# Optimization experiments

Hardware: AMD Instinct MI355X
Metric: run time of the kernel (lower is better)

## Reference

```python
import jax, jax.numpy as jnp
import numpy as np
import math

D = 768      # n_embd
NH = 12      # n_head
L = 4        # n_layer
E = 8        # num_experts
K = 2        # top_k
V = 50257    # vocab
H = 4 * D    # ffn hidden
MOE_LAYERS = (1, 3)


def _ln(x, g, b):
    m = x.mean(-1, keepdims=True)
    v = ((x - m) ** 2).mean(-1, keepdims=True)
    return (x - m) * jax.lax.rsqrt(v + 1e-5) * g + b


def setup_inputs() -> dict:
    key = jax.random.key(0)
    ks = iter(jax.random.split(key, 32))
    s = 0.02

    def rnd(shape):
        return jax.random.normal(next(ks), shape, dtype=jnp.float32) * s

    inp = {
        "x": jax.random.randint(next(ks), (2, 512), 0, V),
        "emb": rnd((V, D)),                       # tied embedding / output projection
        "wqkv": rnd((L, 3 * D, D)), "bqkv": jnp.zeros((L, 3 * D)),
        "wo": rnd((L, D, D)), "bo": jnp.zeros((L, D)),
        "ln1g": jnp.ones((L, D)), "ln1b": jnp.zeros((L, D)),
        "ln2g": jnp.ones((L, D)), "ln2b": jnp.zeros((L, D)),
        "sw1": rnd((2, H, D)), "sb1": jnp.zeros((2, H)),   # dense FFN layers (0, 2)
        "sw2": rnd((2, D, H)), "sb2": jnp.zeros((2, D)),
        "gw": rnd((2, E, D)),                              # router weights (layers 1, 3)
        "mw1": rnd((2, E, H, D)), "mb1": jnp.zeros((2, E, H)),
        "mw2": rnd((2, E, D, H)), "mb2": jnp.zeros((2, E, D)),
        "lnfg": jnp.ones((D,)), "lnfb": jnp.zeros((D,)),
    }
    return inp


def reference(x, emb, wqkv, bqkv, wo, bo, ln1g, ln1b, ln2g, ln2b,
              sw1, sb1, sw2, sb2, gw, mw1, mb1, mw2, mb2, lnfg, lnfb):
    b, t = x.shape
    dh = D // NH

    h = emb[x]  # [b,t,d]
    # sinusoidal positional encoding
    pos = jnp.arange(t, dtype=jnp.float32)[:, None]
    div = jnp.exp(jnp.arange(0, D, 2, dtype=jnp.float32) * (-math.log(10000.0) / D))
    pe = jnp.stack([jnp.sin(pos * div), jnp.cos(pos * div)], axis=-1).reshape(t, D)
    h = h + pe[None]

    # causal mask: query i cannot attend to key j > i
    neg = jnp.asarray(-jnp.inf, dtype=h.dtype)
    mask = jnp.where(jnp.arange(t)[None, :] > jnp.arange(t)[:, None], neg, 0.0)

    std_i = 0
    moe_i = 0
    for i in range(L):
        # pre-norm self-attention
        xn = _ln(h, ln1g[i], ln1b[i])
        qkv = xn @ wqkv[i].T + bqkv[i]          # [b,t,3d]
        q, k, v = jnp.split(qkv, 3, axis=-1)

        def heads(z):
            return z.reshape(b, t, NH, dh).transpose(0, 2, 1, 3)  # [b,nh,t,dh]

        q, k, v = heads(q), heads(k), heads(v)
        sc = jnp.einsum('bhqd,bhkd->bhqk', q, k) / math.sqrt(dh) + mask
        a = jax.nn.softmax(sc, axis=-1)
        o = jnp.einsum('bhqk,bhkd->bhqd', a, v).transpose(0, 2, 1, 3).reshape(b, t, D)
        h = h + o @ wo[i].T + bo[i]

        # pre-norm FFN (dense or MoE)
        xn = _ln(h, ln2g[i], ln2b[i])
        if i in MOE_LAYERS:
            T = b * t
            xf = xn.reshape(T, D)
            gl = xf @ gw[moe_i].T                      # router logits [T,E]
            probs = jax.nn.softmax(gl, axis=-1)
            topv, topi = jax.lax.top_k(probs, K)       # [T,K]
            w = topv / topv.sum(-1, keepdims=True)     # renormalized top-k gates
            cw = jnp.zeros_like(probs).at[jnp.arange(T)[:, None], topi].set(w)  # [T,E]
            he = jax.nn.gelu(jnp.einsum('td,ehd->teh', xf, mw1[moe_i]) + mb1[moe_i],
                             approximate=False)        # [T,E,H]
            ye = jnp.einsum('teh,edh->ted', he, mw2[moe_i]) + mb2[moe_i]        # [T,E,D]
            ff = jnp.einsum('ted,te->td', ye, cw).reshape(b, t, D)
            moe_i += 1
        else:
            ff = jax.nn.gelu(xn @ sw1[std_i].T + sb1[std_i], approximate=False) @ sw2[std_i].T + sb2[std_i]
            std_i += 1
        h = h + ff

    h = _ln(h, lnfg, lnfb)
    logits = h @ emb.T  # tied output projection, [b,t,V]
    return logits
```

## Files before the change

### kernel.cpp

```cpp
#include <hip/hip_runtime.h>
#include <hip/hip_bf16.h>
#include <cstdint>
#include <cstddef>

#define Dm   768
#define NHm  12
#define Lm   4
#define Em   8
#define Vm   50257
#define Hm   3072
#define Tm   512
#define Bm   2
#define NT   (Bm*Tm)
#define NAS  (NT*2)

typedef float f32x4 __attribute__((ext_vector_type(4)));
typedef short bf16x8 __attribute__((ext_vector_type(8)));

__device__ __forceinline__ float gelu_exact(float x) {
    return 0.5f * x * (1.0f + erff(x * 0.70710678118654752440f));
}

__device__ __forceinline__ unsigned short f2bf(float f) {
    __hip_bfloat16 h = __float2bfloat16(f);
// ... 111 lines not shown
    if (valid) {
        const float4* s4 = reinterpret_cast<const float4*>(src);
        #pragma unroll
        for (int q = 0; q < 4; ++q) {
            float4 f = s4[q];
            float vv[4] = {f.x, f.y, f.z, f.w};
            #pragma unroll
            for (int j = 0; j < 4; ++j) {
                int idx = q * 4 + j;
                unsigned short hb = f2bf(vv[j]);
                unsigned short lb = f2bf(vv[j] - bf2f_bits(hb));
                if (idx < 8) { h0.s[idx] = hb; l0.s[idx] = lb; }
                else         { h1.s[idx - 8] = hb; l1.s[idx - 8] = lb; }
            }
        }
    } else {
        h0.v = make_uint4(0,0,0,0); h1.v = make_uint4(0,0,0,0);
        l0.v = make_uint4(0,0,0,0); l1.v = make_uint4(0,0,0,0);
    }
    uint4* dh = reinterpret_cast<uint4*>(&lds_hi[srow * LDT + shalf * 16]);
    dh[0] = h0.v; dh[1] = h1.v;
    uint4* dl = reinterpret_cast<uint4*>(&lds_lo[srow * LDT + shalf * 16]);
    dl[0] = l0.v; dl[1] = l1.v;
}

__device__ __forceinline__ void stage_split_regs(unsigned short* lds_hi,
                                                 unsigned short* lds_lo,
                                                 const float4* rv,
                                                 int srow, int shalf) {
    union { unsigned short s[8]; uint4 v; } h0, h1, l0, l1;
    #pragma unroll
    for (int q = 0; q < 4; ++q) {
        float vv[4] = {rv[q].x, rv[q].y, rv[q].z, rv[q].w};
        #pragma unroll
        for (int j = 0; j < 4; ++j) {
            int idx = q * 4 + j;
            unsigned short hb = f2bf(vv[j]);
            unsigned short lb = f2bf(vv[j] - bf2f_bits(hb));
            if (idx < 8) { h0.s[idx] = hb; l0.s[idx] = lb; }
            else         { h1.s[idx - 8] = hb; l1.s[idx - 8] = lb; }
        }
    }
    uint4* dh = reinterpret_cast<uint4*>(&lds_hi[srow * LDT + shalf * 16]);
    dh[0] = h0.v; dh[1] = h1.v;
    uint4* dl = reinterpret_cast<uint4*>(&lds_lo[srow * LDT + shalf * 16]);
    dl[0] = l0.v; dl[1] = l1.v;
}

__device__ __forceinline__ void stage_tile_copy(unsigned short* lds,
                                                const unsigned short* src,
                                                bool valid, int srow, int shalf) {
    uint4 a0 = make_uint4(0,0,0,0), a1 = make_uint4(0,0,0,0);
    if (valid) {
        a0 = reinterpret_cast<const uint4*>(src)[0];
        a1 = reinterpret_cast<const uint4*>(src)[1];
    }
    uint4* d = reinterpret_cast<uint4*>(&lds[srow * LDT + shalf * 16]);
    d[0] = a0; d[1] = a1;
}

__global__ __launch_bounds__(256) void mfma_gemm_bf(const unsigned short* __restrict__ A,
                                                    const unsigned short* __restrict__ B,
                                                    float* __restrict__ C,
                                                    int M, int N, int K) {
    __shared__ __align__(16) unsigned short SMEM[2 * MB * LDT];
    unsigned short* As = SMEM;
    unsigned short* Bs = SMEM + MB * LDT;
    int tid = threadIdx.x;
    int nt_m = M / MB;
    int total = gridDim.x;
    int bid = blockIdx.x;
    int swz = bid;
    if ((total & 7) == 0) {
        int chunk = total >> 3;
        swz = (bid & 7) * chunk + (bid >> 3);
    }
    int bm = (swz % nt_m) * MB;
    int bn = (swz / nt_m) * NB;
    int srow = tid >> 1, shalf = tid & 1;
    int lane = tid & 63, w = tid >> 6;
    int wr = w >> 1, wc = w & 1;
    int r0 = (lane >> 4) * 4, c0 = lane & 15;
    int kb = (lane >> 4) * 8;

    bool bval = (bn + srow) < N;
    const unsigned short* Ap = A + (size_t)(bm + srow) * K + shalf * 16;
    const unsigned short* Bp = B + (size_t)(bn + srow) * K + shalf * 16;

    uint4 ra0, ra1, rb0, rb1;
    ra0 = reinterpret_cast<const uint4*>(Ap)[0];
    ra1 = reinterpret_cast<const uint4*>(Ap)[1];
    rb0 = make_uint4(0,0,0,0); rb1 = make_uint4(0,0,0,0);
    if (bval) {
        rb0 = reinterpret_cast<const uint4*>(Bp)[0];
        rb1 = reinterpret_cast<const uint4*>(Bp)[1];
    }

    f32x4 acc[4][4] = {};

    for (int kk = 0; kk < K; kk += KB) {
        uint4* da = reinterpret_cast<uint4*>(&As[srow * LDT + shalf * 16]);
        da[0] = ra0; da[1] = ra1;
        uint4* db = reinterpret_cast<uint4*>(&Bs[srow * LDT + shalf * 16]);
        db[0] = rb0; db[1] = rb1;
        __syncthreads();
        if (kk + KB < K) {
            const uint4* na = reinterpret_cast<const uint4*>(Ap + kk + KB);
            ra0 = na[0]; ra1 = na[1];
            if (bval) {
                const uint4* nb = reinterpret_cast<const uint4*>(Bp + kk + KB);
                rb0 = nb[0]; rb1 = nb[1];
            }
        }
        bf16x8 af[4], bf[4];
        #pragma unroll
        for (int m = 0; m < 4; ++m)
            af[m] = *reinterpret_cast<const bf16x8*>(&As[(wr * 64 + m * 16 + c0) * LDT + kb]);
        #pragma unroll
        for (int n = 0; n < 4; ++n)
            bf[n] = *reinterpret_cast<const bf16x8*>(&Bs[(wc * 64 + n * 16 + c0) * LDT + kb]);
        #pragma unroll
        for (int m = 0; m < 4; ++m)
            #pragma unroll
            for (int n = 0; n < 4; ++n)
                acc[m][n] = __builtin_amdgcn_mfma_f32_16x16x32_bf16(af[m], bf[n], acc[m][n], 0, 0, 0);
        __syncthreads();
    }

    float* Ct = reinterpret_cast<float*>(SMEM);
    float* cw = Ct + w * 1024;
    #pragma unroll
    for (int m = 0; m < 4; ++m) {
        #pragma unroll
        for (int n = 0; n < 4; ++n)
            #pragma unroll
            for (int r = 0; r < 4; ++r)
                cw[(r0 + r) * 64 + n * 16 + c0] = acc[m][n][r];
        #pragma unroll
        for (int ch = 0; ch < 4; ++ch) {
            f32x4 vv = *reinterpret_cast<const f32x4*>(&cw[ch * 256 + lane * 4]);
            int rg = bm + wr * 64 + m * 16 + ch * 4 + (lane >> 4);
            int cg = bn + wc * 64 + (lane & 15) * 4;
            if (cg + 3 < N) {
                *reinterpret_cast<f32x4*>(&C[(size_t)rg * N + cg]) = vv;
            } else {
                #pragma unroll
                for (int e = 0; e < 4; ++e)
                    if (cg + e < N) C[(size_t)rg * N + cg + e] = vv[e];
            }
        }
    }
}

__global__ __launch_bounds__(256) void mfma_gemm(const float* __restrict__ A,
                                                 const float* __restrict__ B,
                                                 float* __restrict__ C,
                                                 int M, int N, int K) {
    __shared__ __align__(16) unsigned short As[MB * LDT];
    __shared__ __align__(16) unsigned short Bs[NB * LDT];
    int tid = threadIdx.x;
    int bm = blockIdx.y * MB, bn = blockIdx.x * NB;
    int srow = tid >> 1, shalf = tid & 1;
    int lane = tid & 63, w = tid >> 6;
    int wr = w >> 1, wc = w & 1;
    int r0 = (lane >> 4) * 4, c0 = lane & 15;
    int kb = (lane >> 4) * 8;

    f32x4 acc[4][4] = {};

    for (int kk = 0; kk < K; kk += KB) {
        stage_tile(As, A + (size_t)(bm + srow) * K + kk + shalf * 16, true, srow, shalf);
        bool bval = (bn + srow) < N;
        stage_tile(Bs, B + (size_t)(bn + srow) * K + kk + shalf * 16, bval, srow, shalf);
        __syncthreads();
        bf16x8 af[4], bf[4];
        #pragma unroll
        for (int m = 0; m < 4; ++m)
            af[m] = *reinterpret_cast<const bf16x8*>(&As[(wr * 64 + m * 16 + c0) * LDT + kb]);
        #pragma unroll
        for (int n = 0; n < 4; ++n)
            bf[n] = *reinterpret_cast<const bf16x8*>(&Bs[(wc * 64 + n * 16 + c0) * LDT + kb]);
        #pragma unroll
        for (int m = 0; m < 4; ++m)
            #pragma unroll
            for (int n = 0; n < 4; ++n)
                acc[m][n] = __builtin_amdgcn_mfma_f32_16x16x32_bf16(af[m], bf[n], acc[m][n], 0, 0, 0);
        __syncthreads();
    }

    #pragma unroll
    for (int n = 0; n < 4; ++n) {
        int col = bn + wc * 64 + n * 16 + c0;
        if (col < N) {
            #pragma unroll
            for (int m = 0; m < 4; ++m)
                #pragma unroll
                for (int r = 0; r < 4; ++r) {
                    int row = bm + wr * 64 + m * 16 + r0 + r;
                    C[(size_t)row * N + col] = acc[m][n][r];
                }
        }
    }
}

__global__ __launch_bounds__(256) void mfma_gemm_pA_part(const unsigned short* __restrict__ Ahp,
                                                         const unsigned short* __restrict__ Alp,
                                                         const float* __restrict__ B,
                                                         float* __restrict__ part,
                                                         int M, int N, int K, int KSPLIT) {
    __shared__ __align__(16) unsigned short SMEM[4 * MB * LDT];
    unsigned short* Ah = SMEM;
    unsigned short* Al = SMEM + MB * LDT;
    unsigned short* Bh = SMEM + 2 * MB * LDT;
    unsigned short* Bl = SMEM + 3 * MB * LDT;
    int tid = threadIdx.x;
    int bm = blockIdx.y * MB, bn = blockIdx.x * NB;
    int kc = blockIdx.z;
    int chunk = K / KSPLIT;
    int kbeg = kc * chunk;
    int srow = tid >> 1, shalf = tid & 1;
    int lane = tid & 63, w = tid >> 6;
    int wr = w >> 1, wc = w & 1;
    int r0 = (lane >> 4) * 4, c0 = lane & 15;
    int kb = (lane >> 4) * 8;

    const unsigned short* ApH = Ahp + (size_t)(bm + srow) * K + shalf * 16;
    const unsigned short* ApL = Alp + (size_t)(bm + srow) * K + shalf * 16;
    const float* Bp = B + (size_t)(bn + srow) * K + shalf * 16;

    uint4 rah0 = reinterpret_cast<const uint4*>(ApH + kbeg)[0];
    uint4 rah1 = reinterpret_cast<const uint4*>(ApH + kbeg)[1];
    uint4 ral0 = reinterpret_cast<const uint4*>(ApL + kbeg)[0];
    uint4 ral1 = reinterpret_cast<const uint4*>(ApL + kbeg)[1];
    float4 rbv0 = reinterpret_cast<const float4*>(Bp + kbeg)[0];
    float4 rbv1 = reinterpret_cast<const float4*>(Bp + kbeg)[1];
    float4 rbv2 = reinterpret_cast<const float4*>(Bp + kbeg)[2];
    float4 rbv3 = reinterpret_cast<const float4*>(Bp + kbeg)[3];

    f32x4 acc[4][4] = {};

    for (int kk = kbeg; kk < kbeg + chunk; kk += KB) {
        uint4* dah = reinterpret_cast<uint4*>(&Ah[srow * LDT + shalf * 16]);
        dah[0] = rah0; dah[1] = rah1;
        uint4* dal = reinterpret_cast<uint4*>(&Al[srow * LDT + shalf * 16]);
        dal[0] = ral0; dal[1] = ral1;
        float4 rbv[4] = {rbv0, rbv1, rbv2, rbv3};
        stage_split_regs(Bh, Bl, rbv, srow, shalf);
        __syncthreads();
        if (kk + KB < kbeg + chunk) {
            int kn = kk + KB;
            rah0 = reinterpret_cast<const uint4*>(ApH + kn)[0];
            rah1 = reinterpret_cast<const uint4*>(ApH + kn)[1];
            ral0 = reinterpret_cast<const uint4*>(ApL + kn)[0];
            ral1 = reinterpret_cast<const uint4*>(ApL + kn)[1];
            rbv0 = reinterpret_cast<const float4*>(Bp + kn)[0];
            rbv1 = reinterpret_cast<const float4*>(Bp + kn)[1];
            rbv2 = reinterpret_cast<const float4*>(Bp + kn)[2];
            rbv3 = reinterpret_cast<const float4*>(Bp + kn)[3];
        }
        bf16x8 ah[4], al[4], bh[4], bl[4];
        #pragma unroll
        for (int m = 0; m < 4; ++m) {
            int o = (wr * 64 + m * 16 + c0) * LDT + kb;
            ah[m] = *reinterpret_cast<const bf16x8*>(&Ah[o]);
            al[m] = *reinterpret_cast<const bf16x8*>(&Al[o]);
        }
        #pragma unroll
        for (int n = 0; n < 4; ++n) {
            int o = (wc * 64 + n * 16 + c0) * LDT + kb;
            bh[n] = *reinterpret_cast<const bf16x8*>(&Bh[o]);
            bl[n] = *reinterpret_cast<const bf16x8*>(&Bl[o]);
        }
        #pragma unroll
        for (int m = 0; m < 4; ++m)
            #pragma unroll
            for (int n = 0; n < 4; ++n) {
                acc[m][n] = __builtin_amdgcn_mfma_f32_16x16x32_bf16(al[m], bh[n], acc[m][n], 0, 0, 0);
                acc[m][n] = __builtin_amdgcn_mfma_f32_16x16x32_bf16(ah[m], bl[n], acc[m][n], 0, 0, 0);
                acc[m][n] = __builtin_amdgcn_mfma_f32_16x16x32_bf16(ah[m], bh[n], acc[m][n], 0, 0, 0);
            }
        __syncthreads();
    }

    float* Ct = reinterpret_cast<float*>(SMEM);
    float* cw = Ct + w * 1024;
    float* P = part + (size_t)kc * M * N;
    #pragma unroll
    for (int m = 0; m < 4; ++m) {
        #pragma unroll
        for (int n = 0; n < 4; ++n)
            #pragma unroll
            for (int r = 0; r < 4; ++r)
                cw[(r0 + r) * 64 + n * 16 + c0] = acc[m][n][r];
        #pragma unroll
        for (int ch = 0; ch < 4; ++ch) {
            f32x4 vv = *reinterpret_cast<const f32x4*>(&cw[ch * 256 + lane * 4]);
            int rg = bm + wr * 64 + m * 16 + ch * 4 + (lane >> 4);
            int cg = bn + wc * 64 + (lane & 15) * 4;
            *reinterpret_cast<f32x4*>(&P[(size_t)rg * N + cg]) = vv;
        }
    }
}

__global__ __launch_bounds__(256) void reduce_dense(const float* __restrict__ part,
                                                    const float* __restrict__ bias,
                                                    float* __restrict__ C,
                                                    long MN, int N, int KSPLIT) {
    long stride = (long)gridDim.x * 256 * 4;
    for (long i = ((long)blockIdx.x * 256 + threadIdx.x) * 4; i < MN; i += stride) {
        float4 v = *reinterpret_cast<const float4*>(part + i);
        for (int kc = 1; kc < KSPLIT; ++kc) {
            float4 p = *reinterpret_cast<const float4*>(part + (size_t)kc * MN + i);
            v.x += p.x; v.y += p.y; v.z += p.z; v.w += p.w;
        }
        int col = (int)(i % N);
        float4 b = *reinterpret_cast<const float4*>(bias + col);
        v.x += b.x; v.y += b.y; v.z += b.z; v.w += b.w;
        *reinterpret_cast<float4*>(C + i) = v;
    }
}

__global__ __launch_bounds__(256) void reduce_gelu_bf(const float* __restrict__ part,
                                                      const float* __restrict__ bias,
                                                      unsigned short* __restrict__ outh,
                                                      unsigned short* __restrict__ outl,
                                                      long MN, int N, int KSPLIT) {
    long stride = (long)gridDim.x * 256 * 4;
    for (long i = ((long)blockIdx.x * 256 + threadIdx.x) * 4; i < MN; i += stride) {
        float4 v = *reinterpret_cast<const float4*>(part + i);
        for (int kc = 1; kc < KSPLIT; ++kc) {
            float4 p = *reinterpret_cast<const float4*>(part + (size_t)kc * MN + i);
            v.x += p.x; v.y += p.y; v.z += p.z; v.w += p.w;
        }
        int col = (int)(i % N);
        float4 b = *reinterpret_cast<const float4*>(bias + col);
        float f[4];
        f[0] = gelu_exact(v.x + b.x); f[1] = gelu_exact(v.y + b.y);
        f[2] = gelu_exact(v.z + b.z); f[3] = gelu_exact(v.w + b.w);
        union { unsigned short s[4]; uint2 u; } ph, pl;
        #pragma unroll
        for (int e = 0; e < 4; ++e) {
            unsigned short hb = f2bf(f[e]);
            ph.s[e] = hb;
            pl.s[e] = f2bf(f[e] - bf2f_bits(hb));
        }
        *reinterpret_cast<uint2*>(outh + i) = ph.u;
        *reinterpret_cast<uint2*>(outl + i) = pl.u;
    }
}

__global__ __launch_bounds__(256) void reduce_ln(const float* __restrict__ part,
                                                 const float* __restrict__ bias,
                                                 float* __restrict__ h,
                                                 const float* __restrict__ g,
                                                 const float* __restrict__ b,
                                                 float* __restrict__ xn,
                                                 unsigned short* __restrict__ xnh,
                                                 unsigned short* __restrict__ xnl,
                                                 int KSPLIT) {
    const long MN = (long)NT * Dm;
    int t = blockIdx.x, tid = threadIdx.x;
    float v[3];
    #pragma unroll
    for (int j = 0; j < 3; ++j) {
        int col = tid + j * 256;
        long idx = (long)t * Dm + col;
        float s = part[idx];
        for (int kc = 1; kc < KSPLIT; ++kc) s += part[(size_t)kc * MN + idx];
        s += bias[col] + h[idx];
        h[idx] = s;
        v[j] = s;
    }
    __shared__ float red[256];
    red[tid] = v[0] + v[1] + v[2];
    __syncthreads();
    for (int off = 128; off > 0; off >>= 1) {
        if (tid < off) red[tid] += red[tid + off];
        __syncthreads();
    }
    float mean = red[0] * (1.0f / Dm);
    __syncthreads();
    float d0 = v[0] - mean, d1 = v[1] - mean, d2 = v[2] - mean;
    red[tid] = d0 * d0 + d1 * d1 + d2 * d2;
    __syncthreads();
    for (int off = 128; off > 0; off >>= 1) {
        if (tid < off) red[tid] += red[tid + off];
        __syncthreads();
    }
    float inv = rsqrtf(red[0] * (1.0f / Dm) + 1e-5f);
    float o0 = d0 * inv * g[tid]       + b[tid];
    float o1 = d1 * inv * g[tid + 256] + b[tid + 256];
    float o2 = d2 * inv * g[tid + 512] + b[tid + 512];
    long base = (size_t)t * Dm;
    xn[base + tid] = o0; xn[base + tid + 256] = o1; xn[base + tid + 512] = o2;
    unsigned short h0 = f2bf(o0), h1 = f2bf(o1), h2 = f2bf(o2);
    xnh[base + tid] = h0; xnh[base + tid + 256] = h1; xnh[base + tid + 512] = h2;
    xnl[base + tid]       = f2bf(o0 - bf2f_bits(h0));
    xnl[base + tid + 256] = f2bf(o1 - bf2f_bits(h1));
    xnl[base + tid + 512] = f2bf(o2 - bf2f_bits(h2));
}

__global__ __launch_bounds__(256) void combine_ln(float* __restrict__ h,
                                                  const float* __restrict__ ye,
                                                  const float* __restrict__ g,
                                                  const float* __restrict__ b,
                                                  float* __restrict__ xn,
                                                  unsigned short* __restrict__ xnh,
                                                  unsigned short* __restrict__ xnl) {
    int t = blockIdx.x, tid = threadIdx.x;
    float v[3];
    #pragma unroll
    for (int j = 0; j < 3; ++j) {
        int col = tid + j * 256;
        long idx = (long)t * Dm + col;
        float s = h[idx] + ye[(size_t)(t * 2) * Dm + col] + ye[(size_t)(t * 2 + 1) * Dm + col];
        h[idx] = s;
        v[j] = s;
    }
    __shared__ float red[256];
    red[tid] = v[0] + v[1] + v[2];
    __syncthreads();
    for (int off = 128; off > 0; off >>= 1) {
        if (tid < off) red[tid] += red[tid + off];
        __syncthreads();
    }
    float mean = red[0] * (1.0f / Dm);
    __syncthreads();
    float d0 = v[0] - mean, d1 = v[1] - mean, d2 = v[2] - mean;
    red[tid] = d0 * d0 + d1 * d1 + d2 * d2;
    __syncthreads();
    for (int off = 128; off > 0; off >>= 1) {
        if (tid < off) red[tid] += red[tid + off];
        __syncthreads();
    }
    float inv = rsqrtf(red[0] * (1.0f / Dm) + 1e-5f);
    float o0 = d0 * inv * g[tid]       + b[tid];
    float o1 = d1 * inv * g[tid + 256] + b[tid + 256];
    float o2 = d2 * inv * g[tid + 512] + b[tid + 512];
    long base = (size_t)t * Dm;
    xn[base + tid] = o0; xn[base + tid + 256] = o1; xn[base + tid + 512] = o2;
    unsigned short h0 = f2bf(o0), h1 = f2bf(o1), h2 = f2bf(o2);
    xnh[base + tid] = h0; xnh[base + tid + 256] = h1; xnh[base + tid + 512] = h2;
    xnl[base + tid]       = f2bf(o0 - bf2f_bits(h0));
    xnl[base + tid + 256] = f2bf(o1 - bf2f_bits(h1));
    xnl[base + tid + 512] = f2bf(o2 - bf2f_bits(h2));
}

#define LDA 72
__device__ __forceinline__ void stage16a(unsigned short* dh, unsigned short* dl,
                                         const float* src) {
    union { unsigned short s[8]; uint4 v; } h0, h1, l0, l1;
    const float4* s4 = reinterpret_cast<const float4*>(src);
    #pragma unroll
    for (int q = 0; q < 4; ++q) {
        float4 f = s4[q];
        float vv[4] = {f.x, f.y, f.z, f.w};
        #pragma unroll
        for (int j = 0; j < 4; ++j) {
            int idx = q * 4 + j;
            unsigned short hb = f2bf(vv[j]);
            unsigned short lb = f2bf(vv[j] - bf2f_bits(hb));
            if (idx < 8) { h0.s[idx] = hb; l0.s[idx] = lb; }
            else         { h1.s[idx - 8] = hb; l1.s[idx - 8] = lb; }
        }
    }
    reinterpret_cast<uint4*>(dh)[0] = h0.v; reinterpret_cast<uint4*>(dh)[1] = h1.v;
    reinterpret_cast<uint4*>(dl)[0] = l0.v; reinterpret_cast<uint4*>(dl)[1] = l1.v;
}

__global__ __launch_bounds__(256) void attn_flash(const float* __restrict__ qkv,
                                                  unsigned short* __restrict__ aoh,
                                                  unsigned short* __restrict__ aol) {
    int qt = blockIdx.x;
    int bh = blockIdx.y;
    int b = bh / NHm, hh = bh % NHm;
    const int g0 = b * Tm;
    const int hoff = hh * 64;
    int tid = threadIdx.x;
    int lane = tid & 63, w = tid >> 6;
    int c0 = lane & 15, hi4 = lane >> 4;
    int kb = hi4 * 8;

    __shared__ __align__(16) unsigned short Qh[64 * LDA], Ql[64 * LDA];
    __shared__ __align__(16) unsigned short Kh[64 * LDA], Kl[64 * LDA];
    __shared__ __align__(16) unsigned short Vh[64 * LDA], Vl[64 * LDA];
    __shared__ __align__(16) unsigned short Ph[4][16 * LDA], Pl[4][16 * LDA];

    {
        int srow = tid >> 2, q = tid & 3;
        stage16a(&Qh[srow * LDA + q * 16], &Ql[srow * LDA + q * 16],
                 qkv + (size_t)(g0 + qt * 64 + srow) * (3 * Dm) + hoff + q * 16);
    }
    __syncthreads();

    f32x4 acc_o[4] = {};
    float m_r[4] = {-1e30f, -1e30f, -1e30f, -1e30f};
    float l_r[4] = {0.f, 0.f, 0.f, 0.f};

    for (int kt = 0; kt <= qt; ++kt) {
        {
            int srow = tid >> 2, q = tid & 3;
            stage16a(&Kh[srow * LDA + q * 16], &Kl[srow * LDA + q * 16],
                     qkv + (size_t)(g0 + kt * 64 + srow) * (3 * Dm) + Dm + hoff + q * 16);
        }
        {
            int d = lane, kg = w;
            const float* vbase = qkv + (size_t)(g0 + kt * 64 + kg * 16) * (3 * Dm) + 2 * Dm + hoff + d;
            #pragma unroll
            for (int k2 = 0; k2 < 16; ++k2) {
                float v = vbase[(size_t)k2 * (3 * Dm)];
                unsigned short hb = f2bf(v);
                Vh[d * LDA + kg * 16 + k2] = hb;
                Vl[d * LDA + kg * 16 + k2] = f2bf(v - bf2f_bits(hb));
            }
        }
        __syncthreads();

        f32x4 sAcc[4] = {};
        #pragma unroll
        for (int kk2 = 0; kk2 < 64; kk2 += 32) {
            bf16x8 ah = *reinterpret_cast<const bf16x8*>(&Qh[(w * 16 + c0) * LDA + kk2 + kb]);
            bf16x8 al = *reinterpret_cast<const bf16x8*>(&Ql[(w * 16 + c0) * LDA + kk2 + kb]);
            #pragma unroll
            for (int n = 0; n < 4; ++n) {
                bf16x8 bh_ = *reinterpret_cast<const bf16x8*>(&Kh[(n * 16 + c0) * LDA + kk2 + kb]);
                bf16x8 bl_ = *reinterpret_cast<const bf16x8*>(&Kl[(n * 16 + c0) * LDA + kk2 + kb]);
                sAcc[n] = __builtin_amdgcn_mfma_f32_16x16x32_bf16(al, bh_, sAcc[n], 0, 0, 0);
                sAcc[n] = __builtin_amdgcn_mfma_f32_16x16x32_bf16(ah, bl_, sAcc[n], 0, 0, 0);
                sAcc[n] = __builtin_amdgcn_mfma_f32_16x16x32_bf16(ah, bh_, sAcc[n], 0, 0, 0);
            }
        }

        float p[4][4];
        float smax[4] = {-3e38f, -3e38f, -3e38f, -3e38f};
        #pragma unroll
        for (int n = 0; n < 4; ++n)
            #pragma unroll
            for (int r = 0; r < 4; ++r) {
                float s = sAcc[n][r] * 0.125f;
                if (kt == qt) {
                    int kg = n * 16 + c0;
                    int qg = w * 16 + hi4 * 4 + r;
                    if (kg > qg) s = -3e38f;
                }
                p[n][r] = s;
                smax[r] = fmaxf(smax[r], s);
            }
        #pragma unroll
        for (int off = 1; off < 16; off <<= 1)
            #pragma unroll
            for (int r = 0; r < 4; ++r)
                smax[r] = fmaxf(smax[r], __shfl_xor(smax[r], off));
        float f_r[4], lsum[4];
        #pragma unroll
        for (int r = 0; r < 4; ++r) {
            float mn = fmaxf(m_r[r], smax[r]);
            f_r[r] = expf(m_r[r] - mn);
            m_r[r] = mn;
        }
        #pragma unroll
        for (int n = 0; n < 4; ++n)
            #pragma unroll
            for (int r = 0; r < 4; ++r)
                p[n][r] = expf(p[n][r] - m_r[r]);
        #pragma unroll
        for (int r = 0; r < 4; ++r)
            lsum[r] = p[0][r] + p[1][r] + p[2][r] + p[3][r];
        #pragma unroll
        for (int off = 1; off < 16; off <<= 1)
            #pragma unroll
            for (int r = 0; r < 4; ++r)
                lsum[r] += __shfl_xor(lsum[r], off);
        #pragma unroll
        for (int r = 0; r < 4; ++r)
            l_r[r] = l_r[r] * f_r[r] + lsum[r];
        #pragma unroll
        for (int n = 0; n < 4; ++n)
            #pragma unroll
            for (int r = 0; r < 4; ++r)
                acc_o[n][r] *= f_r[r];

        #pragma unroll
        for (int n = 0; n < 4; ++n)
            #pragma unroll
            for (int r = 0; r < 4; ++r) {
                unsigned short hb = f2bf(p[n][r]);
                int o = (hi4 * 4 + r) * LDA + n * 16 + c0;
                Ph[w][o] = hb;
                Pl[w][o] = f2bf(p[n][r] - bf2f_bits(hb));
            }

        #pragma unroll
        for (int kk2 = 0; kk2 < 64; kk2 += 32) {
            bf16x8 pah = *reinterpret_cast<const bf16x8*>(&Ph[w][c0 * LDA + kk2 + kb]);
            bf16x8 pal = *reinterpret_cast<const bf16x8*>(&Pl[w][c0 * LDA + kk2 + kb]);
            #pragma unroll
            for (int n = 0; n < 4; ++n) {
                bf16x8 vbh = *reinterpret_cast<const bf16x8*>(&Vh[(n * 16 + c0) * LDA + kk2 + kb]);
                bf16x8 vbl = *reinterpret_cast<const bf16x8*>(&Vl[(n * 16 + c0) * LDA + kk2 + kb]);
                acc_o[n] = __builtin_amdgcn_mfma_f32_16x16x32_bf16(pal, vbh, acc_o[n], 0, 0, 0);
                acc_o[n] = __builtin_amdgcn_mfma_f32_16x16x32_bf16(pah, vbl, acc_o[n], 0, 0, 0);
                acc_o[n] = __builtin_amdgcn_mfma_f32_16x16x32_bf16(pah, vbh, acc_o[n], 0, 0, 0);
            }
        }
        __syncthreads();
    }

    float inv[4];
    #pragma unroll
    for (int r = 0; r < 4; ++r) inv[r] = 1.0f / l_r[r];
    #pragma unroll
    for (int n = 0; n < 4; ++n)
        #pragma unroll
        for (int r = 0; r < 4; ++r) {
            int row = g0 + qt * 64 + w * 16 + hi4 * 4 + r;
            float v = acc_o[n][r] * inv[r];
            unsigned short hb = f2bf(v);
            size_t idx = (size_t)row * Dm + hoff + n * 16 + c0;
            aoh[idx] = hb;
            aol[idx] = f2bf(v - bf2f_bits(hb));
        }
}

__global__ __launch_bounds__(256) void router_kernel(const float* __restrict__ xn,
                                                     const float* __restrict__ gw,
                                                     int* __restrict__ topi,
                                                     float* __restrict__ topw) {
    int t = blockIdx.x * 4 + (threadIdx.x >> 6);
    int lane = threadIdx.x & 63;
    const float4* x4 = reinterpret_cast<const float4*>(xn + (size_t)t * Dm);
    float4 xv[3];
    #pragma unroll
    for (int i = 0; i < 3; ++i) xv[i] = x4[lane + i * 64];

    float l[Em];
    #pragma unroll
    for (int e = 0; e < Em; ++e) {
        const float4* w4 = reinterpret_cast<const float4*>(gw + (size_t)e * Dm);
        float dot = 0.f;
        #pragma unroll
        for (int i = 0; i < 3; ++i) {
            float4 wv = w4[lane + i * 64];
            dot += xv[i].x * wv.x + xv[i].y * wv.y + xv[i].z * wv.z + xv[i].w * wv.w;
        }
        #pragma unroll
        for (int off = 32; off > 0; off >>= 1) dot += __shfl_xor(dot, off);
        l[e] = dot;
    }
    if (lane == 0) {
        int i1 = 0;
        #pragma unroll
        for (int e = 1; e < Em; ++e) if (l[e] > l[i1]) i1 = e;
        int i2 = (i1 == 0) ? 1 : 0;
        #pragma unroll
        for (int e = 0; e < Em; ++e) if (e != i1 && l[e] > l[i2]) i2 = e;
        float w1 = 1.0f / (1.0f + expf(l[i2] - l[i1]));
        topi[t * 2] = i1; topi[t * 2 + 1] = i2;
        topw[t * 2] = w1; topw[t * 2 + 1] = 1.0f - w1;
    }
}

__global__ __launch_bounds__(256) void route_build_kernel(const int* __restrict__ topi,
                                                          int* __restrict__ g_cnt,
                                                          int* __restrict__ g_off,
                                                          int* __restrict__ bucket) {
    __shared__ int cnt[Em], off[Em], pos[Em];
    int tid = threadIdx.x;
    if (tid < Em) cnt[tid] = 0;
    __syncthreads();
    for (int ts = tid; ts < NAS; ts += 256) atomicAdd(&cnt[topi[ts]], 1);
    __syncthreads();
    if (tid == 0) {
        int acc = 0;
        for (int e = 0; e < Em; ++e) { off[e] = acc; pos[e] = acc; acc += cnt[e]; }
    }
    __syncthreads();
    for (int ts = tid; ts < NAS; ts += 256) {
        int e = topi[ts];
        int p = atomicAdd(&pos[e], 1);
        bucket[p] = ts;
    }
    if (tid < Em) { g_cnt[tid] = cnt[tid]; g_off[tid] = off[tid]; }
}

template<int SPLIT>
__global__ __launch_bounds__(256) void moe_mfma_gemm1(const unsigned short* __restrict__ xnh,
                                                      const unsigned short* __restrict__ xnl,
                                                      const float* __restrict__ W1all,
                                                      const float* __restrict__ B1all,
                                                      const int* __restrict__ bucket,
                                                      const int* __restrict__ cnt,
                                                      const int* __restrict__ off,
                                                      unsigned short* __restrict__ hegh,
                                                      unsigned short* __restrict__ hegl) {
    int e = blockIdx.z;
    int count = cnt[e];
    int mbase = blockIdx.y * MB;
    if (mbase >= count) return;
    int base = off[e];

    __shared__ __align__(16) unsigned short Ah[MB * LDT];
    __shared__ __align__(16) unsigned short Bh[NB * LDT];
    __shared__ __align__(16) unsigned short Al[SPLIT ? MB * LDT : 8];
    __shared__ __align__(16) unsigned short Bl[SPLIT ? NB * LDT : 8];
    __shared__ int toks[MB];
    int tid = threadIdx.x;
    int bn = blockIdx.x * NB;
    int srow = tid >> 1, shalf = tid & 1;
    int lane = tid & 63, w = tid >> 6;
    int wr = w >> 1, wc = w & 1;
    int r0 = (lane >> 4) * 4, c0 = lane & 15;
    int kb = (lane >> 4) * 8;
    if (tid < MB) {
        int p = mbase + tid;
        toks[tid] = (p < count) ? (bucket[base + p] >> 1) : -1;
    }
    __syncthreads();

    f32x4 acc[4][4] = {};
    const float* W = W1all + (size_t)e * Hm * Dm;
    int t = toks[srow];
    for (int kk = 0; kk < Dm; kk += KB) {
        size_t aoff = (size_t)t * Dm + kk + shalf * 16;
        stage_tile_copy(Ah, xnh + aoff, t >= 0, srow, shalf);
        if (SPLIT) {
            stage_tile_copy(Al, xnl + aoff, t >= 0, srow, shalf);
            stage_tile_split(Bh, Bl, W + (size_t)(bn + srow) * Dm + kk + shalf * 16, true, srow, shalf);
        } else {
            stage_tile(Bh, W + (size_t)(bn + srow) * Dm + kk + shalf * 16, true, srow, shalf);
        }
        __syncthreads();
        bf16x8 ah[4], bh[4], al[4], bl[4];
        #pragma unroll
        for (int m = 0; m < 4; ++m) {
            int o = (wr * 64 + m * 16 + c0) * LDT + kb;
            ah[m] = *reinterpret_cast<const bf16x8*>(&Ah[o]);
            if (SPLIT) al[m] = *reinterpret_cast<const bf16x8*>(&Al[o]);
        }
        #pragma unroll
        for (int n = 0; n < 4; ++n) {
            int o = (wc * 64 + n * 16 + c0) * LDT + kb;
            bh[n] = *reinterpret_cast<const bf16x8*>(&Bh[o]);
            if (SPLIT) bl[n] = *reinterpret_cast<const bf16x8*>(&Bl[o]);
        }
        #pragma unroll
        for (int m = 0; m < 4; ++m)
            #pragma unroll
            for (int n = 0; n < 4; ++n) {
                if (SPLIT) {
                    acc[m][n] = __builtin_amdgcn_mfma_f32_16x16x32_bf16(al[m], bh[n], acc[m][n], 0, 0, 0);
                    acc[m][n] = __builtin_amdgcn_mfma_f32_16x16x32_bf16(ah[m], bl[n], acc[m][n], 0, 0, 0);
                }
                acc[m][n] = __builtin_amdgcn_mfma_f32_16x16x32_bf16(ah[m], bh[n], acc[m][n], 0, 0, 0);
            }
        __syncthreads();
    }

    const float* b1 = B1all + (size_t)e * Hm;
    #pragma unroll
    for (int n = 0; n < 4; ++n) {
        int col = bn + wc * 64 + n * 16 + c0;
        float bv = b1[col];
        #pragma unroll
        for (int m = 0; m < 4; ++m) {
            #pragma unroll
            for (int r = 0; r < 4; ++r) {
                int p = mbase + wr * 64 + m * 16 + r0 + r;
                if (p < count) {
                    float v = gelu_exact(acc[m][n][r] + bv);
                    unsigned short hb = f2bf(v);
                    size_t idx = (size_t)(base + p) * Hm + col;
                    hegh[idx] = hb;
                    hegl[idx] = f2bf(v - bf2f_bits(hb));
                }
            }
        }
    }
}

template<int SPLIT>
__global__ __launch_bounds__(256) void moe_gemm2_part(const unsigned short* __restrict__ hegh,
                                                      const unsigned short* __restrict__ hegl,
                                                      const float* __restrict__ W2all,
                                                      const int* __restrict__ cnt,
                                                      const int* __restrict__ off,
                                                      float* __restrict__ part,
                                                      int KSPLIT) {
    int e = blockIdx.z;
    int count = cnt[e];
    int my = blockIdx.y;
    int kc = my % KSPLIT, mb = my / KSPLIT;
    int mbase = mb * MB;
    if (mbase >= count) return;
    int base = off[e];
    int chunk = Hm / KSPLIT;
    int kbeg = kc * chunk;

    __shared__ __align__(16) unsigned short Ah[MB * LDT];
    __shared__ __align__(16) unsigned short Bh[NB * LDT];
    __shared__ __align__(16) unsigned short Al[SPLIT ? MB * LDT : 8];
    __shared__ __align__(16) unsigned short Bl[SPLIT ? NB * LDT : 8];
    int tid = threadIdx.x;
    int bn = blockIdx.x * NB;
    int srow = tid >> 1, shalf = tid & 1;
    int lane = tid & 63, w = tid >> 6;
    int wr = w >> 1, wc = w & 1;
    int r0 = (lane >> 4) * 4, c0 = lane & 15;
    int kb = (lane >> 4) * 8;

    f32x4 acc[4][4] = {};
    const float* W = W2all + (size_t)e * Dm * Hm;
    bool aval = (mbase + srow) < count;
    for (int kk = kbeg; kk < kbeg + chunk; kk += KB) {
        size_t aoff = (size_t)(base + mbase + srow) * Hm + kk + shalf * 16;
        stage_tile_copy(Ah, hegh + aoff, aval, srow, shalf);
        if (SPLIT) {
            stage_tile_copy(Al, hegl + aoff, aval, srow, shalf);
            stage_tile_split(Bh, Bl, W + (size_t)(bn + srow) * Hm + kk + shalf * 16, true, srow, shalf);
        } else {
            stage_tile(Bh, W + (size_t)(bn + srow) * Hm + kk + shalf * 16, true, srow, shalf);
        }
        __syncthreads();
        bf16x8 ah[4], bh[4], al[4], bl[4];
        #pragma unroll
        for (int m = 0; m < 4; ++m) {
            int o = (wr * 64 + m * 16 + c0) * LDT + kb;
            ah[m] = *reinterpret_cast<const bf16x8*>(&Ah[o]);
            if (SPLIT) al[m] = *reinterpret_cast<const bf16x8*>(&Al[o]);
        }
        #pragma unroll
        for (int n = 0; n < 4; ++n) {
            int o = (wc * 64 + n * 16 + c0) * LDT + kb;
            bh[n] = *reinterpret_cast<const bf16x8*>(&Bh[o]);
            if (SPLIT) bl[n] = *reinterpret_cast<const bf16x8*>(&Bl[o]);
        }
        #pragma unroll
        for (int m = 0; m < 4; ++m)
            #pragma unroll
            for (int n = 0; n < 4; ++n) {
                if (SPLIT) {
                    acc[m][n] = __builtin_amdgcn_mfma_f32_16x16x32_bf16(al[m], bh[n], acc[m][n], 0, 0, 0);
                    acc[m][n] = __builtin_amdgcn_mfma_f32_16x16x32_bf16(ah[m], bl[n], acc[m][n], 0, 0, 0);
                }
                acc[m][n] = __builtin_amdgcn_mfma_f32_16x16x32_bf16(ah[m], bh[n], acc[m][n], 0, 0, 0);
            }
        __syncthreads();
    }

    float* P = part + (size_t)kc * NAS * Dm;
    #pragma unroll
    for (int n = 0; n < 4; ++n) {
        int col = bn + wc * 64 + n * 16 + c0;
        #pragma unroll
        for (int m = 0; m < 4; ++m) {
            #pragma unroll
            for (int r = 0; r < 4; ++r) {
                int p = mbase + wr * 64 + m * 16 + r0 + r;
                if (p < count)
                    P[(size_t)(base + p) * Dm + col] = acc[m][n][r];
            }
        }
    }
}

__global__ __launch_bounds__(256) void moe_reduce(const float* __restrict__ part,
                                                  const float* __restrict__ B2all,
                                                  const int* __restrict__ bucket,
                                                  const int* __restrict__ topi,
                                                  const float* __restrict__ topw,
                                                  float* __restrict__ ye, int KSPLIT) {
    const long MN = (long)NAS * Dm;
    long stride = (long)gridDim.x * 256 * 4;
    for (long i = ((long)blockIdx.x * 256 + threadIdx.x) * 4; i < MN; i += stride) {
        int p = (int)(i / Dm), col = (int)(i % Dm);
        int ts = bucket[p];
        int e = topi[ts];
        float wgt = topw[ts];
        float4 v = *reinterpret_cast<const float4*>(part + i);
        for (int kc = 1; kc < KSPLIT; ++kc) {
            float4 q = *reinterpret_cast<const float4*>(part + (size_t)kc * MN + i);
            v.x += q.x; v.y += q.y; v.z += q.z; v.w += q.w;
        }
        float4 b = *reinterpret_cast<const float4*>(B2all + (size_t)e * Dm + col);
        float4 o;
        o.x = wgt * (v.x + b.x); o.y = wgt * (v.y + b.y);
        o.z = wgt * (v.z + b.z); o.w = wgt * (v.w + b.w);
        *reinterpret_cast<float4*>(ye + (size_t)ts * Dm + col) = o;
    }
}

extern "C" void kernel_launch(void* const* d_in, const int* in_sizes, int n_in,
                              void* d_out, int out_size, void* d_ws, size_t ws_size,
                              hipStream_t stream) {
    const int*   x    = (const int*)d_in[0];
    const float* emb  = (const float*)d_in[1];
    const float* wqkv = (const float*)d_in[2];
    const float* bqkv = (const float*)d_in[3];
    const float* wo   = (const float*)d_in[4];
    const float* bo   = (const float*)d_in[5];
    const float* ln1g = (const float*)d_in[6];
    const float* ln1b = (const float*)d_in[7];
    const float* ln2g = (const float*)d_in[8];
    const float* ln2b = (const float*)d_in[9];
    const float* sw1  = (const float*)d_in[10];
    const float* sb1  = (const float*)d_in[11];
    const float* sw2  = (const float*)d_in[12];
    const float* sb2  = (const float*)d_in[13];
    const float* gw   = (const float*)d_in[14];
    const float* mw1  = (const float*)d_in[15];
    const float* mb1  = (const float*)d_in[16];
    const float* mw2  = (const float*)d_in[17];
    const float* mb2  = (const float*)d_in[18];
    const float* lnfg = (const float*)d_in[19];
    const float* lnfb = (const float*)d_in[20];

    const size_t n_h    = (size_t)NT * Dm;
    const size_t n_qkv  = (size_t)NT * 3 * Dm;
    const size_t n_ye   = (size_t)NAS * Dm;
    const size_t n_part = (size_t)NT * Hm * 2;
    const size_t n_xnb  = (size_t)NT * Dm / 2;
    const size_t n_ffhb = (size_t)NT * Hm / 2;
    const size_t n_hegb = (size_t)NAS * Hm / 2;
    const size_t n_embbf = (size_t)Vm * Dm / 2;
    const size_t n_big = n_h + n_qkv + n_ye + n_part
                       + 2 * n_xnb + 2 * n_xnb
                       + 2 * n_ffhb + 2 * n_hegb;

    size_t wsf = ws_size / sizeof(float);

    float* w = (float*)d_ws;
    float* xn   = w;            w += (size_t)NT * Dm;
    float* topw = w;            w += NAS;
    int*   topi = (int*)w;      w += NAS;
    int*   bucket = (int*)w;    w += NAS;
    int*   e_cnt = (int*)w;     w += 8;
    int*   e_off = (int*)w;     w += 8;
    size_t used = (size_t)(w - (float*)d_ws);

    unsigned short* emb_bf = nullptr;
    if (wsf >= used + n_embbf + 64) {
        emb_bf = (unsigned short*)w;  w += n_embbf;
        used = (size_t)(w - (float*)d_ws);
    }

    float *h, *qkv, *ye, *part;
    unsigned short *xnh, *xnl, *aoh, *aol, *ffhh, *ffhl, *hegh, *hegl;
    float* a;
    bool arena_in_out;
    if (wsf >= used + n_big + 64) { a = w; arena_in_out = false; }
    else                          { a = (float*)d_out; arena_in_out = true; }
    h = a;      a += n_h;
    qkv = a;    a += n_qkv;
    ye = a;     a += n_ye;
    part = a;   a += n_part;
    xnh = (unsigned short*)a;  a += n_xnb;
    xnl = (unsigned short*)a;  a += n_xnb;
    aoh = (unsigned short*)a;  a += n_xnb;
    aol = (unsigned short*)a;  a += n_xnb;
    ffhh = (unsigned short*)a; a += n_ffhb;
    ffhl = (unsigned short*)a; a += n_ffhb;
    hegh = (unsigned short*)a; a += n_hegb;
    hegl = (unsigned short*)a; a += n_hegb;

    if (emb_bf) {
        long n = (long)Vm * Dm;
        cvt_bf16_kernel<<<(unsigned)((n / 8 + 255) / 256), 256, 0, stream>>>(emb, emb_bf, n);
    }

    embed_kernel<<<NT, 256, 0, stream>>>(x, emb, h);
    ln_kernel<<<NT, 256, 0, stream>>>(h, ln1g, ln1b, xn, xnh, xnl);

    const int RBLK = 2048;
    int std_i = 0, moe_i = 0;
    for (int l = 0; l < Lm; ++l) {
        const float* ng = (l < 3) ? (ln1g + (l + 1) * Dm) : lnfg;
        const float* nb = (l < 3) ? (ln1b + (l + 1) * Dm) : lnfb;

        mfma_gemm_pA_part<<<dim3((3 * Dm) / NB, NT / MB, 2), 256, 0, stream>>>(
            xnh, xnl, wqkv + (size_t)l * 3 * Dm * Dm, part, NT, 3 * Dm, Dm, 2);
        reduce_dense<<<RBLK, 256, 0, stream>>>(
            part, bqkv + (size_t)l * 3 * Dm, qkv, (long)NT * 3 * Dm, 3 * Dm, 2);
        attn_flash<<<dim3(Tm / 64, Bm * NHm), 256, 0, stream>>>(qkv, aoh, aol);
        mfma_gemm_pA_part<<<dim3(Dm / NB, NT / MB, 4), 256, 0, stream>>>(
            aoh, aol, wo + (size_t)l * Dm * Dm, part, NT, Dm, Dm, 4);
        reduce_ln<<<NT, 256, 0, stream>>>(
            part, bo + (size_t)l * Dm, h, ln2g + l * Dm, ln2b + l * Dm, xn, xnh, xnl, 4);

        if (l == 1 || l == 3) {
            router_kernel<<<NT / 4, 256, 0, stream>>>(
                xn, gw + (size_t)moe_i * Em * Dm, topi, topw);
            route_build_kernel<<<1, 256, 0, stream>>>(topi, e_cnt, e_off, bucket);
            if (l == 3) {
                moe_mfma_gemm1<0><<<dim3(Hm / NB, NAS / MB, Em), 256, 0, stream>>>(
                    xnh, xnl, mw1 + (size_t)moe_i * Em * Hm * Dm, mb1 + (size_t)moe_i * Em * Hm,
                    bucket, e_cnt, e_off, hegh, hegl);
                moe_gemm2_part<0><<<dim3(Dm / NB, (NAS / MB) * 4, Em), 256, 0, stream>>>(
                    hegh, hegl, mw2 + (size_t)moe_i * Em * Dm * Hm, e_cnt, e_off, part, 4);
            } else {
                moe_mfma_gemm1<1><<<dim3(Hm / NB, NAS / MB, Em), 256, 0, stream>>>(
                    xnh, xnl, mw1 + (size_t)moe_i * Em * Hm * Dm, mb1 + (size_t)moe_i * Em * Hm,
                    bucket, e_cnt, e_off, hegh, hegl);
                moe_gemm2_part<1><<<dim3(Dm / NB, (NAS / MB) * 4, Em), 256, 0, stream>>>(
                    hegh, hegl, mw2 + (size_t)moe_i * Em * Dm * Hm, e_cnt, e_off, part, 4);
            }
            moe_reduce<<<RBLK, 256, 0, stream>>>(
                part, mb2 + (size_t)moe_i * Em * Dm, bucket, topi, topw, ye, 4);
            combine_ln<<<NT, 256, 0, stream>>>(h, ye, ng, nb, xn, xnh, xnl);
            moe_i++;
        } else {
            mfma_gemm_pA_part<<<dim3(Hm / NB, NT / MB, 2), 256, 0, stream>>>(
                xnh, xnl, sw1 + (size_t)std_i * Hm * Dm, part, NT, Hm, Dm, 2);
            reduce_gelu_bf<<<RBLK, 256, 0, stream>>>(
                part, sb1 + (size_t)std_i * Hm, ffhh, ffhl, (long)NT * Hm, Hm, 2);
            mfma_gemm_pA_part<<<dim3(Dm / NB, NT / MB, 8), 256, 0, stream>>>(
                ffhh, ffhl, sw2 + (size_t)std_i * Dm * Hm, part, NT, Dm, Hm, 8);
            reduce_ln<<<NT, 256, 0, stream>>>(
                part, sb2 + (size_t)std_i * Dm, h, ng, nb, xn, xnh, xnl, 8);
            std_i++;
        }
    }

    if (emb_bf && !arena_in_out) {
        int nblk = (NT / MB) * ((Vm + NB - 1) / NB);
        mfma_gemm_bf<<<dim3(nblk), 256, 0, stream>>>(
            xnh, emb_bf, (float*)d_out, NT, Vm, Dm);
    } else {
        mfma_gemm<<<dim3((Vm + NB - 1) / NB, NT / MB), 256, 0, stream>>>(
            xn, emb, (float*)d_out, NT, Vm, Dm);
    }
}
```

Baseline: 1.024 ms.

## Fuse split-K reductions into attention staging and MoE combine+layernorm

The split-K partial sum plus bias for QKV is now computed directly while attention stages Q/K/V tiles, which removes the reduce_dense kernel and the qkv intermediate buffer. The MoE reduce kernel is also folded into the combine+layernorm kernel, using a new inverse routing map built in route_build, which removes the ye buffer. This saves two launches per layer and the global round trips for the intermediates. In exchange, attention re-reads both K partials for every query tile, so K/V reads are doubled and repeated across tiles, and the MoE gather becomes scalar rather than float4.

```diff
diff --git a/kernel.cpp b/kernel.cpp
--- a/kernel.cpp
+++ b/kernel.cpp
@@ -437,24 +437,6 @@
     }
 }
 
-__global__ __launch_bounds__(256) void reduce_dense(const float* __restrict__ part,
-                                                    const float* __restrict__ bias,
-                                                    float* __restrict__ C,
-                                                    long MN, int N, int KSPLIT) {
-    long stride = (long)gridDim.x * 256 * 4;
-    for (long i = ((long)blockIdx.x * 256 + threadIdx.x) * 4; i < MN; i += stride) {
-        float4 v = *reinterpret_cast<const float4*>(part + i);
-        for (int kc = 1; kc < KSPLIT; ++kc) {
-            float4 p = *reinterpret_cast<const float4*>(part + (size_t)kc * MN + i);
-            v.x += p.x; v.y += p.y; v.z += p.z; v.w += p.w;
-        }
-        int col = (int)(i % N);
-        float4 b = *reinterpret_cast<const float4*>(bias + col);
-        v.x += b.x; v.y += b.y; v.z += b.z; v.w += b.w;
-        *reinterpret_cast<float4*>(C + i) = v;
-    }
-}
-
 __global__ __launch_bounds__(256) void reduce_gelu_bf(const float* __restrict__ part,
                                                       const float* __restrict__ bias,
                                                       unsigned short* __restrict__ outh,
@@ -535,20 +517,43 @@
     xnl[base + tid + 512] = f2bf(o2 - bf2f_bits(h2));
 }
 
-__global__ __launch_bounds__(256) void combine_ln(float* __restrict__ h,
-                                                  const float* __restrict__ ye,
-                                                  const float* __restrict__ g,
-                                                  const float* __restrict__ b,
-                                                  float* __restrict__ xn,
-                                                  unsigned short* __restrict__ xnh,
-                                                  unsigned short* __restrict__ xnl) {
+__global__ __launch_bounds__(256) void moe_combine_ln(float* __restrict__ h,
+                                                      const float* __restrict__ part,
+                                                      const float* __restrict__ B2all,
+                                                      const int* __restrict__ inv,
+                                                      const int* __restrict__ topi,
+                                                      const float* __restrict__ topw,
+                                                      const float* __restrict__ g,
+                                                      const float* __restrict__ b,
+                                                      float* __restrict__ xn,
+                                                      unsigned short* __restrict__ xnh,
+                                                      unsigned short* __restrict__ xnl,
+                                                      int KSPLIT) {
+    const long MN = (long)NAS * Dm;
     int t = blockIdx.x, tid = threadIdx.x;
+    int ts0 = t * 2, ts1 = t * 2 + 1;
+    int pos0 = inv[ts0], pos1 = inv[ts1];
+    int e0 = topi[ts0], e1 = topi[ts1];
+    float w0 = topw[ts0], w1 = topw[ts1];
+
     float v[3];
     #pragma unroll
     for (int j = 0; j < 3; ++j) {
         int col = tid + j * 256;
         long idx = (long)t * Dm + col;
-        float s = h[idx] + ye[(size_t)(t * 2) * Dm + col] + ye[(size_t)(t * 2 + 1) * Dm + col];
+        float s = h[idx];
+        {
+            float vv = part[(size_t)pos0 * Dm + col];
+            for (int kc = 1; kc < KSPLIT; ++kc)
+                vv += part[(size_t)kc * MN + (size_t)pos0 * Dm + col];
+            s += w0 * (vv + B2all[(size_t)e0 * Dm + col]);
+        }
+        {
+            float vv = part[(size_t)pos1 * Dm + col];
+            for (int kc = 1; kc < KSPLIT; ++kc)
+                vv += part[(size_t)kc * MN + (size_t)pos1 * Dm + col];
+            s += w1 * (vv + B2all[(size_t)e1 * Dm + col]);
+        }
         h[idx] = s;
         v[j] = s;
     }
@@ -568,10 +573,10 @@
         if (tid < off) red[tid] += red[tid + off];
         __syncthreads();
     }
-    float inv = rsqrtf(red[0] * (1.0f / Dm) + 1e-5f);
-    float o0 = d0 * inv * g[tid]       + b[tid];
-    float o1 = d1 * inv * g[tid + 256] + b[tid + 256];
-    float o2 = d2 * inv * g[tid + 512] + b[tid + 512];
+    float inv2 = rsqrtf(red[0] * (1.0f / Dm) + 1e-5f);
+    float o0 = d0 * inv2 * g[tid]       + b[tid];
+    float o1 = d1 * inv2 * g[tid + 256] + b[tid + 256];
+    float o2 = d2 * inv2 * g[tid + 512] + b[tid + 512];
     long base = (size_t)t * Dm;
     xn[base + tid] = o0; xn[base + tid + 256] = o1; xn[base + tid + 512] = o2;
     unsigned short h0 = f2bf(o0), h1 = f2bf(o1), h2 = f2bf(o2);
@@ -582,14 +587,22 @@
 }
 
 #define LDA 72
-__device__ __forceinline__ void stage16a(unsigned short* dh, unsigned short* dl,
-                                         const float* src) {
+#define QKVN (3 * Dm)
+__device__ __forceinline__ void stage16a_sum(unsigned short* dh, unsigned short* dl,
+                                             const float* s0, const float* s1,
+                                             const float* bias) {
     union { unsigned short s[8]; uint4 v; } h0, h1, l0, l1;
-    const float4* s4 = reinterpret_cast<const float4*>(src);
+    const float4* a4 = reinterpret_cast<const float4*>(s0);
+    const float4* b4 = reinterpret_cast<const float4*>(s1);
+    const float4* c4 = reinterpret_cast<const float4*>(bias);
     #pragma unroll
     for (int q = 0; q < 4; ++q) {
-        float4 f = s4[q];
-        float vv[4] = {f.x, f.y, f.z, f.w};
+        float4 fa = a4[q], fb = b4[q], fc = c4[q];
+        float vv[4];
+        vv[0] = fa.x + fb.x + fc.x;
+        vv[1] = fa.y + fb.y + fc.y;
+        vv[2] = fa.z + fb.z + fc.z;
+        vv[3] = fa.w + fb.w + fc.w;
         #pragma unroll
         for (int j = 0; j < 4; ++j) {
             int idx = q * 4 + j;
@@ -603,9 +616,11 @@
     reinterpret_cast<uint4*>(dl)[0] = l0.v; reinterpret_cast<uint4*>(dl)[1] = l1.v;
 }
 
-__global__ __launch_bounds__(256) void attn_flash(const float* __restrict__ qkv,
+__global__ __launch_bounds__(256) void attn_flash(const float* __restrict__ part,
+                                                  const float* __restrict__ bqkv,
                                                   unsigned short* __restrict__ aoh,
                                                   unsigned short* __restrict__ aol) {
+    const long MN2 = (long)NT * QKVN;
     int qt = blockIdx.x;
     int bh = blockIdx.y;
     int b = bh / NHm, hh = bh % NHm;
@@ -623,8 +638,9 @@
 
     {
         int srow = tid >> 2, q = tid & 3;
-        stage16a(&Qh[srow * LDA + q * 16], &Ql[srow * LDA + q * 16],
-                 qkv + (size_t)(g0 + qt * 64 + srow) * (3 * Dm) + hoff + q * 16);
+        const float* s0 = part + (size_t)(g0 + qt * 64 + srow) * QKVN + hoff + q * 16;
+        stage16a_sum(&Qh[srow * LDA + q * 16], &Ql[srow * LDA + q * 16],
+                     s0, s0 + MN2, bqkv + hoff + q * 16);
     }
     __syncthreads();
 
@@ -632,18 +648,21 @@
     float m_r[4] = {-1e30f, -1e30f, -1e30f, -1e30f};
     float l_r[4] = {0.f, 0.f, 0.f, 0.f};
 
+    float bv_v = bqkv[2 * Dm + hoff + lane];
+
     for (int kt = 0; kt <= qt; ++kt) {
         {
             int srow = tid >> 2, q = tid & 3;
-            stage16a(&Kh[srow * LDA + q * 16], &Kl[srow * LDA + q * 16],
-                     qkv + (size_t)(g0 + kt * 64 + srow) * (3 * Dm) + Dm + hoff + q * 16);
+            const float* s0 = part + (size_t)(g0 + kt * 64 + srow) * QKVN + Dm + hoff + q * 16;
+            stage16a_sum(&Kh[srow * LDA + q * 16], &Kl[srow * LDA + q * 16],
+                         s0, s0 + MN2, bqkv + Dm + hoff + q * 16);
         }
         {
             int d = lane, kg = w;
-            const float* vbase = qkv + (size_t)(g0 + kt * 64 + kg * 16) * (3 * Dm) + 2 * Dm + hoff + d;
+            const float* vb0 = part + (size_t)(g0 + kt * 64 + kg * 16) * QKVN + 2 * Dm + hoff + d;
             #pragma unroll
             for (int k2 = 0; k2 < 16; ++k2) {
-                float v = vbase[(size_t)k2 * (3 * Dm)];
+                float v = vb0[(size_t)k2 * QKVN] + vb0[MN2 + (size_t)k2 * QKVN] + bv_v;
                 unsigned short hb = f2bf(v);
                 Vh[d * LDA + kg * 16 + k2] = hb;
                 Vl[d * LDA + kg * 16 + k2] = f2bf(v - bf2f_bits(hb));
@@ -798,7 +817,8 @@
 __global__ __launch_bounds__(256) void route_build_kernel(const int* __restrict__ topi,
                                                           int* __restrict__ g_cnt,
                                                           int* __restrict__ g_off,
-                                                          int* __restrict__ bucket) {
+                                                          int* __restrict__ bucket,
+                                                          int* __restrict__ invmap) {
     __shared__ int cnt[Em], off[Em], pos[Em];
     int tid = threadIdx.x;
     if (tid < Em) cnt[tid] = 0;
@@ -814,6 +834,7 @@
         int e = topi[ts];
         int p = atomicAdd(&pos[e], 1);
         bucket[p] = ts;
+        invmap[ts] = p;
     }
     if (tid < Em) { g_cnt[tid] = cnt[tid]; g_off[tid] = off[tid]; }
 }
@@ -995,32 +1016,6 @@
                     P[(size_t)(base + p) * Dm + col] = acc[m][n][r];
             }
         }
-    }
-}
-
-__global__ __launch_bounds__(256) void moe_reduce(const float* __restrict__ part,
-                                                  const float* __restrict__ B2all,
-                                                  const int* __restrict__ bucket,
-                                                  const int* __restrict__ topi,
-                                                  const float* __restrict__ topw,
-                                                  float* __restrict__ ye, int KSPLIT) {
-    const long MN = (long)NAS * Dm;
-    long stride = (long)gridDim.x * 256 * 4;
-    for (long i = ((long)blockIdx.x * 256 + threadIdx.x) * 4; i < MN; i += stride) {
-        int p = (int)(i / Dm), col = (int)(i % Dm);
-        int ts = bucket[p];
-        int e = topi[ts];
-        float wgt = topw[ts];
-        float4 v = *reinterpret_cast<const float4*>(part + i);
-        for (int kc = 1; kc < KSPLIT; ++kc) {
-            float4 q = *reinterpret_cast<const float4*>(part + (size_t)kc * MN + i);
-            v.x += q.x; v.y += q.y; v.z += q.z; v.w += q.w;
-        }
-        float4 b = *reinterpret_cast<const float4*>(B2all + (size_t)e * Dm + col);
-        float4 o;
-        o.x = wgt * (v.x + b.x); o.y = wgt * (v.y + b.y);
-        o.z = wgt * (v.z + b.z); o.w = wgt * (v.w + b.w);
-        *reinterpret_cast<float4*>(ye + (size_t)ts * Dm + col) = o;
     }
 }
 
@@ -1068,6 +1063,7 @@
     float* topw = w;            w += NAS;
     int*   topi = (int*)w;      w += NAS;
     int*   bucket = (int*)w;    w += NAS;
+    int*   invmap = (int*)w;    w += NAS;
     int*   e_cnt = (int*)w;     w += 8;
     int*   e_off = (int*)w;     w += 8;
     size_t used = (size_t)(w - (float*)d_ws);
@@ -1078,16 +1074,16 @@
         used = (size_t)(w - (float*)d_ws);
     }
 
-    float *h, *qkv, *ye, *part;
+    float *h, *qkv_unused, *ye_unused, *part;
     unsigned short *xnh, *xnl, *aoh, *aol, *ffhh, *ffhl, *hegh, *hegl;
     float* a;
     bool arena_in_out;
     if (wsf >= used + n_big + 64) { a = w; arena_in_out = false; }
     else                          { a = (float*)d_out; arena_in_out = true; }
-    h = a;      a += n_h;
-    qkv = a;    a += n_qkv;
-    ye = a;     a += n_ye;
-    part = a;   a += n_part;
+    h = a;          a += n_h;
+    qkv_unused = a; a += n_qkv;
+    ye_unused = a;  a += n_ye;
+    part = a;       a += n_part;
     xnh = (unsigned short*)a;  a += n_xnb;
     xnl = (unsigned short*)a;  a += n_xnb;
     aoh = (unsigned short*)a;  a += n_xnb;
@@ -1096,6 +1092,7 @@
     ffhl = (unsigned short*)a; a += n_ffhb;
     hegh = (unsigned short*)a; a += n_hegb;
     hegl = (unsigned short*)a; a += n_hegb;
+    (void)qkv_unused; (void)ye_unused;
 
     if (emb_bf) {
         long n = (long)Vm * Dm;
@@ -1113,9 +1110,8 @@
 
         mfma_gemm_pA_part<<<dim3((3 * Dm) / NB, NT / MB, 2), 256, 0, stream>>>(
             xnh, xnl, wqkv + (size_t)l * 3 * Dm * Dm, part, NT, 3 * Dm, Dm, 2);
-        reduce_dense<<<RBLK, 256, 0, stream>>>(
-            part, bqkv + (size_t)l * 3 * Dm, qkv, (long)NT * 3 * Dm, 3 * Dm, 2);
-        attn_flash<<<dim3(Tm / 64, Bm * NHm), 256, 0, stream>>>(qkv, aoh, aol);
+        attn_flash<<<dim3(Tm / 64, Bm * NHm), 256, 0, stream>>>(
+            part, bqkv + (size_t)l * 3 * Dm, aoh, aol);
         mfma_gemm_pA_part<<<dim3(Dm / NB, NT / MB, 4), 256, 0, stream>>>(
             aoh, aol, wo + (size_t)l * Dm * Dm, part, NT, Dm, Dm, 4);
         reduce_ln<<<NT, 256, 0, stream>>>(
@@ -1124,7 +1120,7 @@
         if (l == 1 || l == 3) {
             router_kernel<<<NT / 4, 256, 0, stream>>>(
                 xn, gw + (size_t)moe_i * Em * Dm, topi, topw);
-            route_build_kernel<<<1, 256, 0, stream>>>(topi, e_cnt, e_off, bucket);
+            route_build_kernel<<<1, 256, 0, stream>>>(topi, e_cnt, e_off, bucket, invmap);
             if (l == 3) {
                 moe_mfma_gemm1<0><<<dim3(Hm / NB, NAS / MB, Em), 256, 0, stream>>>(
                     xnh, xnl, mw1 + (size_t)moe_i * Em * Hm * Dm, mb1 + (size_t)moe_i * Em * Hm,
@@ -1138,9 +1134,9 @@
                 moe_gemm2_part<1><<<dim3(Dm / NB, (NAS / MB) * 4, Em), 256, 0, stream>>>(
                     hegh, hegl, mw2 + (size_t)moe_i * Em * Dm * Hm, e_cnt, e_off, part, 4);
             }
-            moe_reduce<<<RBLK, 256, 0, stream>>>(
-                part, mb2 + (size_t)moe_i * Em * Dm, bucket, topi, topw, ye, 4);
-            combine_ln<<<NT, 256, 0, stream>>>(h, ye, ng, nb, xn, xnh, xnl);
+            moe_combine_ln<<<NT, 256, 0, stream>>>(
+                h, part, mb2 + (size_t)moe_i * Em * Dm, invmap, topi, topw,
+                ng, nb, xn, xnh, xnl, 4);
             moe_i++;
         } else {
             mfma_gemm_pA_part<<<dim3(Hm / NB, NT / MB, 2), 256, 0, stream>>>(
```

New measurement: 1.032 ms. No clear change (+0.9%).
